# Kernel tuning notes

Hardware: AMD Instinct MI355X
Metric: run time of the kernel (lower is better)

## Reference

```python
import jax, jax.numpy as jnp
import numpy as np

IN_F = 2048
OUT_F = 2048
BATCH = 16384
BASE_SPARSITY = 0.02
REVIVAL_DENSITY = 0.2   # rows for dead ('low') output neurons
RELIEF_DENSITY = 0.15   # cols for saturated ('high') input neurons
DEAD = np.arange(16)                      # 'low' extrema (row indices)
SATURATED = np.arange(100, 900, 100)      # 'high' extrema (col indices)


def _make_mask(key):
    k1, k2, k3 = jax.random.split(key, 3)
    base = (jax.random.uniform(k1, (OUT_F, IN_F)) < BASE_SPARSITY).astype(jnp.float32)
    patch = jnp.zeros((OUT_F, IN_F), jnp.float32)
    # dense-ish rows for dead output neurons
    row_patch = (jax.random.uniform(k2, (len(DEAD), IN_F)) < REVIVAL_DENSITY).astype(jnp.float32)
    patch = patch.at[jnp.asarray(DEAD), :].set(row_patch)
    # dense-ish cols for saturated input neurons (overwrite, matching torch order)
    col_patch = (jax.random.uniform(k3, (OUT_F, len(SATURATED))) < RELIEF_DENSITY).astype(jnp.float32)
    patch = patch.at[:, jnp.asarray(SATURATED)].set(col_patch)
    return jnp.maximum(base, patch)


def setup_inputs() -> dict:
    key = jax.random.key(0)
    kx, kw, km = jax.random.split(key, 3)
    x = jax.random.normal(kx, (BATCH, IN_F), dtype=jnp.float32)
    # kaiming_uniform_(a=sqrt(5)) -> U(-bound, bound), bound = sqrt(6/((1+a^2)*fan_in)) = 1/sqrt(fan_in)
    bound = 1.0 / np.sqrt(IN_F)
    weight = jax.random.uniform(kw, (OUT_F, IN_F), minval=-bound, maxval=bound, dtype=jnp.float32)
    bias = jnp.zeros((OUT_F,), jnp.float32)
    mask = _make_mask(km)
    return {"x": x, "weight": weight, "bias": bias, "mask": mask}


def reference(x, weight, bias, mask):
    # F.linear(x, weight * mask, bias): y = x @ (W*M)^T + b
    return jnp.einsum('bi,oi->bo', x, weight * mask) + bias
```

## Files before the change

### kernel.cpp

```cpp
#include <hip/hip_runtime.h>
#include <stdint.h>

#define BATCH 16384
#define IN_F 2048
#define OUT_F 2048

typedef unsigned short u16;
typedef __attribute__((ext_vector_type(8))) short bf16x8;
typedef __attribute__((ext_vector_type(4))) float f32x4;

__device__ __forceinline__ u16 f2bf(float f) {
  union { float f; uint32_t u; } v; v.f = f;
  uint32_t u = v.u;
  u += 0x7FFFu + ((u >> 16) & 1u);
  return (u16)(u >> 16);
}


__global__ void cvt_fused(const float4* __restrict__ x, const float4* __restrict__ w,
                          const float4* __restrict__ m, u16* __restrict__ xb,
                          u16* __restrict__ wb) {
  const int NX = BATCH * IN_F / 4;
  int i = blockIdx.x * 256 + threadIdx.x;
  if (i < NX) {
    float4 v = x[i];
    uint2 p;
    p.x = (uint32_t)f2bf(v.x) | ((uint32_t)f2bf(v.y) << 16);
    p.y = (uint32_t)f2bf(v.z) | ((uint32_t)f2bf(v.w) << 16);
    ((uint2*)xb)[i] = p;
  } else {
    int j = i - NX;
    float4 wv = w[j];
    float4 mv = m[j];
    uint2 p;
    p.x = (uint32_t)f2bf(wv.x * mv.x) | ((uint32_t)f2bf(wv.y * mv.y) << 16);
    p.y = (uint32_t)f2bf(wv.z * mv.z) | ((uint32_t)f2bf(wv.w * mv.w) << 16);
    ((uint2*)wb)[j] = p;
  }
}


__device__ __forceinline__ void async_cp16(const void* g, void* l) {
  __builtin_amdgcn_global_load_lds(
      (const __attribute__((address_space(1))) void*)g,
      (__attribute__((address_space(3))) void*)l,
      16, 0, 0);
}


#define BK 32
#define NT (IN_F / BK)

__global__ __launch_bounds__(512, 2) void gemm_bf16(const u16* __restrict__ A,
                                                    const u16* __restrict__ B,
                                                    const float* __restrict__ bias,
                                                    float* __restrict__ C) {
  __shared__ __align__(128) char smem[4 * 32768];
  const int K = IN_F, N = OUT_F;
  const int tid = threadIdx.x;
  const int lane = tid & 63, wave = tid >> 6;
  const int wm = wave >> 2;
  const int wn = wave & 3;
  const long bn = (long)blockIdx.x * 256;
  const long bm = (long)blockIdx.y * 256;

  const int sr = tid >> 2, sc = tid & 3;
  const int scs = sc ^ ((sr >> 1) & 3);
  const u16* gA = A + (bm + sr) * K + scs * 8;
  const u16* gB = B + (bn + sr) * K + scs * 8;
  const long hiK = 128L * K;
  const int ldst = tid * 16;

  auto stageA = [&](int slot, int kt) {
    char* sb = smem + slot * 32768;
    const long ko = (long)kt * BK;
    async_cp16(gA + ko, sb + ldst);
    async_cp16(gA + hiK + ko, sb + 8192 + ldst);
  };
  auto stageB = [&](int slot, int kt) {
    char* sb = smem + slot * 32768 + 16384;
    const long ko = (long)kt * BK;
    async_cp16(gB + ko, sb + ldst);
    async_cp16(gB + hiK + ko, sb + 8192 + ldst);
  };

  const int rl = lane & 15;
  const int q = lane >> 4;
  const int fb = rl * 64 + ((q ^ ((rl >> 1) & 3)) * 16);

  f32x4 acc[8][4];
#pragma unroll
  for (int i = 0; i < 8; i++)
#pragma unroll
    for (int j = 0; j < 4; j++)
#pragma unroll
      for (int r = 0; r < 4; r++) acc[i][j][r] = 0.0f;

  stageA(0, 0); stageB(0, 0);
  stageA(1, 1); stageB(1, 1);
  stageA(2, 2); stageB(2, 2);
  asm volatile("s_waitcnt vmcnt(8)" ::: "memory");
  __builtin_amdgcn_s_barrier();
  __builtin_amdgcn_sched_barrier(0);

  for (int t = 0; t < NT; ++t) {
    const int slot = t & 3;
    const int kt3 = (t + 3 < NT) ? t + 3 : NT - 1;
    const int s3 = (t + 3) & 3;
    const char* sA = smem + slot * 32768 + wm * 8192;
    const char* sB = smem + slot * 32768 + 16384 + wn * 4096;

    bf16x8 af0[4], af1[4], bf[4];
#pragma unroll
    for (int i = 0; i < 4; i++) af0[i] = *(const bf16x8*)(sA + i * 1024 + fb);
#pragma unroll
    for (int j = 0; j < 4; j++) bf[j] = *(const bf16x8*)(sB + j * 1024 + fb);
    stageA(s3, kt3);
    __builtin_amdgcn_s_barrier();
    __builtin_amdgcn_s_setprio(1);
#pragma unroll
    for (int i = 0; i < 4; i++)
#pragma unroll
      for (int j = 0; j < 4; j++)
        acc[i][j] = __builtin_amdgcn_mfma_f32_16x16x32_bf16(af0[i], bf[j], acc[i][j], 0, 0, 0);
    __builtin_amdgcn_s_setprio(0);
    __builtin_amdgcn_s_barrier();

#pragma unroll
    for (int i = 0; i < 4; i++) af1[i] = *(const bf16x8*)(sA + 4096 + i * 1024 + fb);
    stageB(s3, kt3);
    __builtin_amdgcn_s_barrier();
    __builtin_amdgcn_s_setprio(1);
#pragma unroll
    for (int i = 0; i < 4; i++)
#pragma unroll
      for (int j = 0; j < 4; j++)
        acc[4 + i][j] = __builtin_amdgcn_mfma_f32_16x16x32_bf16(af1[i], bf[j], acc[4 + i][j], 0, 0, 0);
    __builtin_amdgcn_s_setprio(0);
    asm volatile("s_waitcnt vmcnt(8)" ::: "memory");
    __builtin_amdgcn_s_barrier();
    __builtin_amdgcn_sched_barrier(0);
  }

  asm volatile("s_waitcnt vmcnt(0)" ::: "memory");

  const int cn = lane & 15;
  const int crow = (lane >> 4) * 4;
#pragma unroll
  for (int j = 0; j < 4; j++) {
    const long n = bn + wn * 64 + j * 16 + cn;
    const float bv = bias[n];
#pragma unroll
    for (int i = 0; i < 8; i++) {
      const long m0 = bm + wm * 128 + i * 16 + crow;
      float* cp = C + m0 * N + n;
#pragma unroll
      for (int r = 0; r < 4; r++)
        cp[(long)r * N] = acc[i][j][r] + bv;
    }
  }
}


__global__ void naive_kernel(const float* __restrict__ x, const float* __restrict__ w,
                             const float* __restrict__ bias, const float* __restrict__ m,
                             float* __restrict__ out) {
  size_t idx = (size_t)blockIdx.x * 256 + threadIdx.x;
  int o = (int)(idx % OUT_F);
  size_t b = idx / OUT_F;
  float s = bias[o];
  const float* xr = x + b * IN_F;
  const float* wr = w + (size_t)o * IN_F;
  const float* mr = m + (size_t)o * IN_F;
  for (int k = 0; k < IN_F; k++) s += xr[k] * wr[k] * mr[k];
  out[idx] = s;
}

extern "C" void kernel_launch(void* const* d_in, const int* in_sizes, int n_in,
                              void* d_out, int out_size, void* d_ws, size_t ws_size,
                              hipStream_t stream) {
  const float* x = (const float*)d_in[0];
  const float* w = (const float*)d_in[1];
  const float* bias = (const float*)d_in[2];
  const float* mask = (const float*)d_in[3];
  float* out = (float*)d_out;

  const size_t xb_elems = (size_t)BATCH * IN_F;
  const size_t wm_elems = (size_t)OUT_F * IN_F;
  const size_t need = (xb_elems + wm_elems) * sizeof(u16);

  if (ws_size >= need) {
    u16* xb = (u16*)d_ws;
    u16* wm = xb + xb_elems;
    const uint32_t nblk = (uint32_t)((xb_elems + wm_elems) / 4 / 256);
    cvt_fused<<<nblk, 256, 0, stream>>>((const float4*)x, (const float4*)w,
                                        (const float4*)mask, xb, wm);
    gemm_bf16<<<dim3(OUT_F / 256, BATCH / 256), 512, 0, stream>>>(xb, wm, bias, out);
  } else {
    naive_kernel<<<(uint32_t)(((size_t)BATCH * OUT_F) / 256), 256, 0, stream>>>(x, w, bias, mask, out);
  }
}
```

Measured before the change: 371.4 us.

## Cut per-tile barriers and double-buffer LDS fragments in registers across k-tiles

Result: faster. 360.6 us (-2.9%).

```diff
diff --git a/kernel.cpp b/kernel.cpp
--- a/kernel.cpp
+++ b/kernel.cpp
@@ -87,6 +87,8 @@
   const int rl = lane & 15;
   const int q = lane >> 4;
   const int fb = rl * 64 + ((q ^ ((rl >> 1) & 3)) * 16);
+  const int aoff = wm * 8192;
+  const int boff = 16384 + wn * 4096;
 
   f32x4 acc[8][4];
 #pragma unroll
@@ -99,48 +101,55 @@
   stageA(0, 0); stageB(0, 0);
   stageA(1, 1); stageB(1, 1);
   stageA(2, 2); stageB(2, 2);
-  asm volatile("s_waitcnt vmcnt(8)" ::: "memory");
+  asm volatile("s_waitcnt vmcnt(4)" ::: "memory");
   __builtin_amdgcn_s_barrier();
-  __builtin_amdgcn_sched_barrier(0);
-
-  for (int t = 0; t < NT; ++t) {
-    const int slot = t & 3;
-    const int kt3 = (t + 3 < NT) ? t + 3 : NT - 1;
-    const int s3 = (t + 3) & 3;
-    const char* sA = smem + slot * 32768 + wm * 8192;
-    const char* sB = smem + slot * 32768 + 16384 + wn * 4096;
-
-    bf16x8 af0[4], af1[4], bf[4];
-#pragma unroll
-    for (int i = 0; i < 4; i++) af0[i] = *(const bf16x8*)(sA + i * 1024 + fb);
-#pragma unroll
-    for (int j = 0; j < 4; j++) bf[j] = *(const bf16x8*)(sB + j * 1024 + fb);
-    stageA(s3, kt3);
-    __builtin_amdgcn_s_barrier();
-    __builtin_amdgcn_s_setprio(1);
-#pragma unroll
-    for (int i = 0; i < 4; i++)
-#pragma unroll
-      for (int j = 0; j < 4; j++)
-        acc[i][j] = __builtin_amdgcn_mfma_f32_16x16x32_bf16(af0[i], bf[j], acc[i][j], 0, 0, 0);
-    __builtin_amdgcn_s_setprio(0);
-    __builtin_amdgcn_s_barrier();
-
-#pragma unroll
-    for (int i = 0; i < 4; i++) af1[i] = *(const bf16x8*)(sA + 4096 + i * 1024 + fb);
-    stageB(s3, kt3);
-    __builtin_amdgcn_s_barrier();
-    __builtin_amdgcn_s_setprio(1);
-#pragma unroll
-    for (int i = 0; i < 4; i++)
-#pragma unroll
-      for (int j = 0; j < 4; j++)
-        acc[4 + i][j] = __builtin_amdgcn_mfma_f32_16x16x32_bf16(af1[i], bf[j], acc[4 + i][j], 0, 0, 0);
-    __builtin_amdgcn_s_setprio(0);
-    asm volatile("s_waitcnt vmcnt(8)" ::: "memory");
-    __builtin_amdgcn_s_barrier();
-    __builtin_amdgcn_sched_barrier(0);
-  }
+
+  bf16x8 afA[4], bfA[4], afB[4], bfB[4];
+#pragma unroll
+  for (int i = 0; i < 4; i++) afA[i] = *(const bf16x8*)(smem + aoff + i * 1024 + fb);
+#pragma unroll
+  for (int j = 0; j < 4; j++) bfA[j] = *(const bf16x8*)(smem + boff + j * 1024 + fb);
+
+#define BODY(T, curA, curB, nxtA, nxtB)                                          \
+  do {                                                                           \
+    const int t_ = (T);                                                          \
+    const int slot_ = t_ & 3, s1_ = (t_ + 1) & 3, s3_ = (t_ + 3) & 3;            \
+    const int kt3_ = (t_ + 3 < NT) ? t_ + 3 : NT - 1;                            \
+    const char* sA_ = smem + slot_ * 32768 + aoff;                               \
+    const char* sA1_ = smem + s1_ * 32768 + aoff;                                \
+    const char* sB1_ = smem + s1_ * 32768 + boff;                                \
+    stageA(s3_, kt3_);                                                           \
+    stageB(s3_, kt3_);                                                           \
+    bf16x8 af1_[4];                                                              \
+    _Pragma("unroll")                                                            \
+    for (int i = 0; i < 4; i++) af1_[i] = *(const bf16x8*)(sA_ + 4096 + i * 1024 + fb); \
+    __builtin_amdgcn_s_setprio(1);                                               \
+    _Pragma("unroll")                                                            \
+    for (int i = 0; i < 4; i++)                                                  \
+      _Pragma("unroll")                                                          \
+      for (int j = 0; j < 4; j++)                                                \
+        acc[i][j] = __builtin_amdgcn_mfma_f32_16x16x32_bf16(curA[i], curB[j], acc[i][j], 0, 0, 0); \
+    __builtin_amdgcn_s_setprio(0);                                               \
+    _Pragma("unroll")                                                            \
+    for (int i = 0; i < 4; i++) nxtA[i] = *(const bf16x8*)(sA1_ + i * 1024 + fb); \
+    _Pragma("unroll")                                                            \
+    for (int j = 0; j < 4; j++) nxtB[j] = *(const bf16x8*)(sB1_ + j * 1024 + fb); \
+    __builtin_amdgcn_s_setprio(1);                                               \
+    _Pragma("unroll")                                                            \
+    for (int i = 0; i < 4; i++)                                                  \
+      _Pragma("unroll")                                                          \
+      for (int j = 0; j < 4; j++)                                                \
+        acc[4 + i][j] = __builtin_amdgcn_mfma_f32_16x16x32_bf16(af1_[i], curB[j], acc[4 + i][j], 0, 0, 0); \
+    __builtin_amdgcn_s_setprio(0);                                               \
+    asm volatile("s_waitcnt vmcnt(4)" ::: "memory");                             \
+    __builtin_amdgcn_s_barrier();                                                \
+  } while (0)
+
+  for (int t = 0; t < NT; t += 2) {
+    BODY(t, afA, bfA, afB, bfB);
+    BODY(t + 1, afB, bfB, afA, bfA);
+  }
+#undef BODY
 
   asm volatile("s_waitcnt vmcnt(0)" ::: "memory");
 
```
